# Performance work log

Measured on AMD Instinct MI355X. Metric: run time of the kernel, lower is better.

The kernel has to match this reference:

```python
import jax, jax.numpy as jnp
import numpy as np

B, N = 16384, 64

def setup_inputs() -> dict:
    key = jax.random.key(0)
    a = jax.random.normal(key, (B, N, N), dtype=jnp.float32)
    # symeig / eigh require symmetric input; symmetrize like SPD inputs would be
    x = 0.5 * (a + jnp.swapaxes(a, -2, -1))
    return {"input": x}

def reference(input) -> jnp.ndarray:
    # s, u = symeig(input); out = u @ diag(exp(s)) @ u^T
    s, u = jnp.linalg.eigh(input)          # s: [B,N], u: [B,N,N]
    # fuse diag_embed + two matmuls: (u * exp(s)) @ u^T
    return jnp.einsum('bik,bk,bjk->bij', u, jnp.exp(s), u)
```

## Files before the change

### kernel.cpp

```cpp
#include <hip/hip_runtime.h>
#include <math.h>

#define NB 64
#define TPB 256

__device__ __constant__ float CF[16] = {
    1.0f,
    1.0f,
    0.5f,
    1.6666666666666666e-01f,
    4.1666666666666664e-02f,
    8.3333333333333332e-03f,
    1.3888888888888889e-03f,
    1.9841269841269841e-04f,
    2.4801587301587302e-05f,
    2.7557319223985893e-06f,
    2.7557319223985888e-07f,
    2.5052108385441720e-08f,
    2.0876756987868100e-09f,
    1.6059043836821613e-10f,
    1.1470745597729725e-11f,
    7.6471637318198164e-13f
};

typedef __attribute__((ext_vector_type(8))) short bf16x8;
typedef __attribute__((ext_vector_type(16))) float f32x16;
typedef __attribute__((ext_vector_type(4))) unsigned int u32x4;

#define MFMA32 __builtin_amdgcn_mfma_f32_32x32x16_bf16
#define BCH(x) __builtin_bit_cast(bf16x8, x)

__device__ __forceinline__ void split_pk(float x0, float x1, unsigned& ph, unsigned& pl) {
    unsigned h;
    asm("v_cvt_pk_bf16_f32 %0, %1, %2" : "=v"(h) : "v"(x0), "v"(x1));
    float h0 = __builtin_bit_cast(float, h << 16);
    float h1 = __builtin_bit_cast(float, h & 0xFFFF0000u);
    float r0 = x0 - h0;
    float r1 = x1 - h1;
    unsigned l;
    asm("v_cvt_pk_bf16_f32 %0, %1, %2" : "=v"(l) : "v"(r0), "v"(r1));
    ph = h; pl = l;
}

__device__ __forceinline__ void pswap(unsigned& a, unsigned& b, int lh) {
#if __has_builtin(__builtin_amdgcn_permlane32_swap)
    auto r = __builtin_amdgcn_permlane32_swap((int)a, (int)b, false, false);
    a = (unsigned)r[0];
    b = (unsigned)r[1];
#else
    unsigned pa = (unsigned)__shfl_xor((int)a, 32);
    unsigned pb = (unsigned)__shfl_xor((int)b, 32);
    unsigned o0 = lh ? pb : a;
    unsigned o1 = lh ? b : pa;
    a = o0; b = o1;
#endif
}

__device__ __forceinline__ void tile_to_op(const float* v, int lh, u32x4* fh, u32x4* fl) {
    unsigned Wh[4][2], Wl[4][2];
#pragma unroll
    for (int g = 0; g < 4; ++g) {
        split_pk(v[g * 4 + 0], v[g * 4 + 1], Wh[g][0], Wl[g][0]);
        split_pk(v[g * 4 + 2], v[g * 4 + 3], Wh[g][1], Wl[g][1]);
    }
#pragma unroll
    for (int p = 0; p < 2; ++p) {
        unsigned a0 = Wh[2 * p][0], b0 = Wh[2 * p + 1][0];
        unsigned a1 = Wh[2 * p][1], b1 = Wh[2 * p + 1][1];
        pswap(a0, b0, lh);
        pswap(a1, b1, lh);
        fh[p] = (u32x4){a0, a1, b0, b1};
        a0 = Wl[2 * p][0]; b0 = Wl[2 * p + 1][0];
        a1 = Wl[2 * p][1]; b1 = Wl[2 * p + 1][1];
        pswap(a0, b0, lh);
        pswap(a1, b1, lh);
        fl[p] = (u32x4){a0, a1, b0, b1};
    }
}

__device__ __forceinline__ f32x16 mm3v(const u32x4* ah, const u32x4* al,
                                       const u32x4* bh, const u32x4* bl) {
    f32x16 acc = {};
#pragma unroll
    for (int f = 0; f < 4; ++f) acc = MFMA32(BCH(ah[f]), BCH(bh[f]), acc, 0, 0, 0);
#pragma unroll
    for (int f = 0; f < 4; ++f) acc = MFMA32(BCH(al[f]), BCH(bh[f]), acc, 0, 0, 0);
#pragma unroll
    for (int f = 0; f < 4; ++f) acc = MFMA32(BCH(ah[f]), BCH(bl[f]), acc, 0, 0, 0);
    return acc;
}

__device__ __forceinline__ void wr_tile(float* __restrict__ out, size_t base,
                                        int C, int R, int l31, int lh, const float* w) {
    float* rowp = out + base + (size_t)(C * 32 + l31) * NB + R * 32 + 4 * lh;
#pragma unroll
    for (int g = 0; g < 4; ++g) {
        float4 v = make_float4(w[g * 4 + 0], w[g * 4 + 1], w[g * 4 + 2], w[g * 4 + 3]);
        *reinterpret_cast<float4*>(rowp + 8 * g) = v;
    }
}

__global__ __launch_bounds__(TPB, 2)
void spd_expmap_reg(const float* __restrict__ in, float* __restrict__ out)
{
    const int tid  = threadIdx.x;
    const int lane = tid & 63;
    const int wv   = tid >> 6;
    const int l31 = lane & 31;
    const int lh  = lane >> 5;
    const size_t base = ((size_t)blockIdx.x * 4 + wv) * (NB * NB);
    const float* rp0 = in + base + (size_t)l31 * NB;
    const float* rp1 = rp0 + (size_t)32 * NB;

    unsigned dmask = 0;
#pragma unroll
    for (int g = 0; g < 4; ++g)
#pragma unroll
        for (int q = 0; q < 4; ++q)
            if (4 * lh + 8 * g + q == l31) dmask |= 1u << (g * 4 + q);

    u32x4 XH[2][4], XL[2][4];
#pragma unroll
    for (int R = 0; R < 2; ++R) {
        const float* rp = R ? rp1 : rp0;
#pragma unroll
        for (int f = 0; f < 4; ++f) {
            const float* q = rp + 16 * f + 8 * lh;
            float4 a = *reinterpret_cast<const float4*>(q);
            float4 b = *reinterpret_cast<const float4*>(q + 4);
            unsigned h0, l0, h1, l1, h2, l2, h3, l3;
            split_pk(a.x, a.y, h0, l0);
            split_pk(a.z, a.w, h1, l1);
            split_pk(b.x, b.y, h2, l2);
            split_pk(b.z, b.w, h3, l3);
            XH[R][f] = (u32x4){h0, h1, h2, h3};
            XL[R][f] = (u32x4){l0, l1, l2, l3};
        }
    }

    float x00[16], x10[16], x01[16], x11[16];
#pragma unroll
    for (int g = 0; g < 4; ++g) {
        float4 t;
        t = *reinterpret_cast<const float4*>(rp0 + 4 * lh + 8 * g);
        x00[g*4+0] = t.x; x00[g*4+1] = t.y; x00[g*4+2] = t.z; x00[g*4+3] = t.w;
        t = *reinterpret_cast<const float4*>(rp0 + 32 + 4 * lh + 8 * g);
        x10[g*4+0] = t.x; x10[g*4+1] = t.y; x10[g*4+2] = t.z; x10[g*4+3] = t.w;
        t = *reinterpret_cast<const float4*>(rp1 + 4 * lh + 8 * g);
        x01[g*4+0] = t.x; x01[g*4+1] = t.y; x01[g*4+2] = t.z; x01[g*4+3] = t.w;
        t = *reinterpret_cast<const float4*>(rp1 + 32 + 4 * lh + 8 * g);
        x11[g*4+0] = t.x; x11[g*4+1] = t.y; x11[g*4+2] = t.z; x11[g*4+3] = t.w;
    }

    f32x16 a00 = mm3v(XH[0], XL[0], XH[0], XL[0]);
    f32x16 a01 = mm3v(XH[0], XL[0], XH[1], XL[1]);
    f32x16 a10 = mm3v(XH[1], XL[1], XH[0], XL[0]);
    f32x16 a11 = mm3v(XH[1], XL[1], XH[1], XL[1]);

    float fr = 0.f;
#pragma unroll
    for (int r = 0; r < 16; ++r)
        fr += a00[r]*a00[r] + a01[r]*a01[r] + a10[r]*a10[r] + a11[r]*a11[r];
#pragma unroll
    for (int off = 32; off; off >>= 1) fr += __shfl_xor(fr, off);

    const float bound = sqrtf(sqrtf(fr));
    int sexp = 0;
    if (bound > 4.f) {
        sexp = (int)ceilf(log2f(bound)) - 2;
        if (sexp < 0) sexp = 0;
        if (sexp > 24) sexp = 24;
    }
    const float sc1 = exp2f(-(float)sexp);
    const float sc2 = sc1 * sc1;

#pragma unroll
    for (int r = 0; r < 16; ++r) { x00[r] *= sc1; x10[r] *= sc1; x01[r] *= sc1; x11[r] *= sc1; }

    u32x4 YH[2][4], YL[2][4];
    {
        float v[16];
#pragma unroll
        for (int r = 0; r < 16; ++r) v[r] = a00[r] * sc2;
        tile_to_op(v, lh, &YH[0][0], &YL[0][0]);
#pragma unroll
        for (int r = 0; r < 16; ++r) v[r] = a10[r] * sc2;
        tile_to_op(v, lh, &YH[0][2], &YL[0][2]);
#pragma unroll
        for (int r = 0; r < 16; ++r) v[r] = a01[r] * sc2;
        tile_to_op(v, lh, &YH[1][0], &YL[1][0]);
#pragma unroll
        for (int r = 0; r < 16; ++r) v[r] = a11[r] * sc2;
        tile_to_op(v, lh, &YH[1][2], &YL[1][2]);
    }

    u32x4 PH[2][4], PL[2][4];
    {
        float v[16];
#pragma unroll
        for (int r = 0; r < 16; ++r)
            v[r] = CF[13] * x00[r] + (((dmask >> r) & 1) ? CF[12] : 0.f);
        tile_to_op(v, lh, &PH[0][0], &PL[0][0]);
#pragma unroll
        for (int r = 0; r < 16; ++r) v[r] = CF[13] * x10[r];
        tile_to_op(v, lh, &PH[0][2], &PL[0][2]);
#pragma unroll
        for (int r = 0; r < 16; ++r) v[r] = CF[13] * x01[r];
        tile_to_op(v, lh, &PH[1][0], &PL[1][0]);
#pragma unroll
        for (int r = 0; r < 16; ++r)
            v[r] = CF[13] * x11[r] + (((dmask >> r) & 1) ? CF[12] : 0.f);
        tile_to_op(v, lh, &PH[1][2], &PL[1][2]);
    }

#pragma unroll 1
    for (int j = 5; j >= 0; --j) {
        const float cI = CF[2 * j], cX = CF[2 * j + 1];
        const bool last = (j == 0) && (sexp == 0);
        {
            f32x16 t0 = mm3v(YH[0], YL[0], PH[0], PL[0]);
            f32x16 t1 = mm3v(YH[1], YL[1], PH[0], PL[0]);
            float w0[16], w1[16];
#pragma unroll
            for (int r = 0; r < 16; ++r) {
                w0[r] = fmaf(cX, x00[r], t0[r]) + (((dmask >> r) & 1) ? cI : 0.f);
                w1[r] = fmaf(cX, x10[r], t1[r]);
            }
            if (last) {
                wr_tile(out, base, 0, 0, l31, lh, w0);
                wr_tile(out, base, 0, 1, l31, lh, w1);
            } else {
                tile_to_op(w0, lh, &PH[0][0], &PL[0][0]);
                tile_to_op(w1, lh, &PH[0][2], &PL[0][2]);
            }
        }
        {
            f32x16 t0 = mm3v(YH[0], YL[0], PH[1], PL[1]);
            f32x16 t1 = mm3v(YH[1], YL[1], PH[1], PL[1]);
            float w0[16], w1[16];
#pragma unroll
            for (int r = 0; r < 16; ++r) {
                w0[r] = fmaf(cX, x01[r], t0[r]);
                w1[r] = fmaf(cX, x11[r], t1[r]) + (((dmask >> r) & 1) ? cI : 0.f);
            }
            if (last) {
                wr_tile(out, base, 1, 0, l31, lh, w0);
                wr_tile(out, base, 1, 1, l31, lh, w1);
            } else {
                tile_to_op(w0, lh, &PH[1][0], &PL[1][0]);
                tile_to_op(w1, lh, &PH[1][2], &PL[1][2]);
            }
        }
    }

#pragma unroll 1
    for (int t = 0; t < sexp; ++t) {
        f32x16 s00 = mm3v(PH[0], PL[0], PH[0], PL[0]);
        f32x16 s01 = mm3v(PH[0], PL[0], PH[1], PL[1]);
        f32x16 s10 = mm3v(PH[1], PL[1], PH[0], PL[0]);
        f32x16 s11 = mm3v(PH[1], PL[1], PH[1], PL[1]);
        float w[16];
        if (t == sexp - 1) {
#pragma unroll
            for (int r = 0; r < 16; ++r) w[r] = s00[r];
            wr_tile(out, base, 0, 0, l31, lh, w);
#pragma unroll
            for (int r = 0; r < 16; ++r) w[r] = s10[r];
            wr_tile(out, base, 0, 1, l31, lh, w);
#pragma unroll
            for (int r = 0; r < 16; ++r) w[r] = s01[r];
            wr_tile(out, base, 1, 0, l31, lh, w);
#pragma unroll
            for (int r = 0; r < 16; ++r) w[r] = s11[r];
            wr_tile(out, base, 1, 1, l31, lh, w);
        } else {
#pragma unroll
            for (int r = 0; r < 16; ++r) w[r] = s00[r];
            tile_to_op(w, lh, &PH[0][0], &PL[0][0]);
#pragma unroll
            for (int r = 0; r < 16; ++r) w[r] = s10[r];
            tile_to_op(w, lh, &PH[0][2], &PL[0][2]);
#pragma unroll
            for (int r = 0; r < 16; ++r) w[r] = s01[r];
            tile_to_op(w, lh, &PH[1][0], &PL[1][0]);
#pragma unroll
            for (int r = 0; r < 16; ++r) w[r] = s11[r];
            tile_to_op(w, lh, &PH[1][2], &PL[1][2]);
        }
    }
}

extern "C" void kernel_launch(void* const* d_in, const int* in_sizes, int n_in,
                              void* d_out, int out_size, void* d_ws, size_t ws_size,
                              hipStream_t stream) {
    const float* in = reinterpret_cast<const float*>(d_in[0]);
    float* out = reinterpret_cast<float*>(d_out);
    const int nmat = in_sizes[0] / (NB * NB);
    hipLaunchKernelGGL(spd_expmap_reg, dim3(nmat / 4), dim3(TPB), 0, stream, in, out);
}
```

Before: 278.5 us.

## Re-read input tiles from global memory instead of holding them in registers

Drops the 64 persistent registers that held the scaled input matrix X and reloads X tiles from global memory (expected to hit cache) each time they are needed in the Taylor loop. The X² tiles are stored unscaled, and the scale factors are folded into the FMA coefficients so the pre-scaling passes disappear. Launch bounds rise from 2 to 3 blocks per CU to turn the lower register pressure into occupancy. The cost is repeated global loads inside the Horner loop and a risk of spills under the tighter register cap.

```diff
diff --git a/kernel.cpp b/kernel.cpp
--- a/kernel.cpp
+++ b/kernel.cpp
@@ -100,7 +100,16 @@
     }
 }
 
-__global__ __launch_bounds__(TPB, 2)
+__device__ __forceinline__ void load_x(const float* rp, int colbase, float* xr) {
+#pragma unroll
+    for (int g = 0; g < 4; ++g) {
+        float4 t = *reinterpret_cast<const float4*>(rp + colbase + 8 * g);
+        xr[g * 4 + 0] = t.x; xr[g * 4 + 1] = t.y;
+        xr[g * 4 + 2] = t.z; xr[g * 4 + 3] = t.w;
+    }
+}
+
+__global__ __launch_bounds__(TPB, 3)
 void spd_expmap_reg(const float* __restrict__ in, float* __restrict__ out)
 {
     const int tid  = threadIdx.x;
@@ -138,29 +147,27 @@
         }
     }
 
-    float x00[16], x10[16], x01[16], x11[16];
-#pragma unroll
-    for (int g = 0; g < 4; ++g) {
-        float4 t;
-        t = *reinterpret_cast<const float4*>(rp0 + 4 * lh + 8 * g);
-        x00[g*4+0] = t.x; x00[g*4+1] = t.y; x00[g*4+2] = t.z; x00[g*4+3] = t.w;
-        t = *reinterpret_cast<const float4*>(rp0 + 32 + 4 * lh + 8 * g);
-        x10[g*4+0] = t.x; x10[g*4+1] = t.y; x10[g*4+2] = t.z; x10[g*4+3] = t.w;
-        t = *reinterpret_cast<const float4*>(rp1 + 4 * lh + 8 * g);
-        x01[g*4+0] = t.x; x01[g*4+1] = t.y; x01[g*4+2] = t.z; x01[g*4+3] = t.w;
-        t = *reinterpret_cast<const float4*>(rp1 + 32 + 4 * lh + 8 * g);
-        x11[g*4+0] = t.x; x11[g*4+1] = t.y; x11[g*4+2] = t.z; x11[g*4+3] = t.w;
-    }
-
-    f32x16 a00 = mm3v(XH[0], XL[0], XH[0], XL[0]);
-    f32x16 a01 = mm3v(XH[0], XL[0], XH[1], XL[1]);
-    f32x16 a10 = mm3v(XH[1], XL[1], XH[0], XL[0]);
-    f32x16 a11 = mm3v(XH[1], XL[1], XH[1], XL[1]);
-
+    u32x4 YH[2][4], YL[2][4];
     float fr = 0.f;
-#pragma unroll
-    for (int r = 0; r < 16; ++r)
-        fr += a00[r]*a00[r] + a01[r]*a01[r] + a10[r]*a10[r] + a11[r]*a11[r];
+    {
+        f32x16 t;
+        t = mm3v(XH[0], XL[0], XH[0], XL[0]);
+#pragma unroll
+        for (int r = 0; r < 16; ++r) fr += t[r] * t[r];
+        tile_to_op((const float*)&t, lh, &YH[0][0], &YL[0][0]);
+        t = mm3v(XH[1], XL[1], XH[0], XL[0]);
+#pragma unroll
+        for (int r = 0; r < 16; ++r) fr += t[r] * t[r];
+        tile_to_op((const float*)&t, lh, &YH[0][2], &YL[0][2]);
+        t = mm3v(XH[0], XL[0], XH[1], XL[1]);
+#pragma unroll
+        for (int r = 0; r < 16; ++r) fr += t[r] * t[r];
+        tile_to_op((const float*)&t, lh, &YH[1][0], &YL[1][0]);
+        t = mm3v(XH[1], XL[1], XH[1], XL[1]);
+#pragma unroll
+        for (int r = 0; r < 16; ++r) fr += t[r] * t[r];
+        tile_to_op((const float*)&t, lh, &YH[1][2], &YL[1][2]);
+    }
 #pragma unroll
     for (int off = 32; off; off >>= 1) fr += __shfl_xor(fr, off);
 
@@ -174,82 +181,67 @@
     const float sc1 = exp2f(-(float)sexp);
     const float sc2 = sc1 * sc1;
 
-#pragma unroll
-    for (int r = 0; r < 16; ++r) { x00[r] *= sc1; x10[r] *= sc1; x01[r] *= sc1; x11[r] *= sc1; }
-
-    u32x4 YH[2][4], YL[2][4];
-    {
-        float v[16];
-#pragma unroll
-        for (int r = 0; r < 16; ++r) v[r] = a00[r] * sc2;
-        tile_to_op(v, lh, &YH[0][0], &YL[0][0]);
-#pragma unroll
-        for (int r = 0; r < 16; ++r) v[r] = a10[r] * sc2;
-        tile_to_op(v, lh, &YH[0][2], &YL[0][2]);
-#pragma unroll
-        for (int r = 0; r < 16; ++r) v[r] = a01[r] * sc2;
-        tile_to_op(v, lh, &YH[1][0], &YL[1][0]);
-#pragma unroll
-        for (int r = 0; r < 16; ++r) v[r] = a11[r] * sc2;
-        tile_to_op(v, lh, &YH[1][2], &YL[1][2]);
-    }
-
     u32x4 PH[2][4], PL[2][4];
     {
-        float v[16];
+        const float c13s = CF[13] * sc1;
+        float xr[16], w[16];
+        load_x(rp0, 4 * lh, xr);
 #pragma unroll
         for (int r = 0; r < 16; ++r)
-            v[r] = CF[13] * x00[r] + (((dmask >> r) & 1) ? CF[12] : 0.f);
-        tile_to_op(v, lh, &PH[0][0], &PL[0][0]);
-#pragma unroll
-        for (int r = 0; r < 16; ++r) v[r] = CF[13] * x10[r];
-        tile_to_op(v, lh, &PH[0][2], &PL[0][2]);
-#pragma unroll
-        for (int r = 0; r < 16; ++r) v[r] = CF[13] * x01[r];
-        tile_to_op(v, lh, &PH[1][0], &PL[1][0]);
+            w[r] = fmaf(c13s, xr[r], (((dmask >> r) & 1) ? CF[12] : 0.f));
+        tile_to_op(w, lh, &PH[0][0], &PL[0][0]);
+        load_x(rp0, 32 + 4 * lh, xr);
+#pragma unroll
+        for (int r = 0; r < 16; ++r) w[r] = c13s * xr[r];
+        tile_to_op(w, lh, &PH[0][2], &PL[0][2]);
+        load_x(rp1, 4 * lh, xr);
+#pragma unroll
+        for (int r = 0; r < 16; ++r) w[r] = c13s * xr[r];
+        tile_to_op(w, lh, &PH[1][0], &PL[1][0]);
+        load_x(rp1, 32 + 4 * lh, xr);
 #pragma unroll
         for (int r = 0; r < 16; ++r)
-            v[r] = CF[13] * x11[r] + (((dmask >> r) & 1) ? CF[12] : 0.f);
-        tile_to_op(v, lh, &PH[1][2], &PL[1][2]);
+            w[r] = fmaf(c13s, xr[r], (((dmask >> r) & 1) ? CF[12] : 0.f));
+        tile_to_op(w, lh, &PH[1][2], &PL[1][2]);
     }
 
 #pragma unroll 1
     for (int j = 5; j >= 0; --j) {
-        const float cI = CF[2 * j], cX = CF[2 * j + 1];
+        const float cI = CF[2 * j], cXs = CF[2 * j + 1] * sc1;
         const bool last = (j == 0) && (sexp == 0);
         {
             f32x16 t0 = mm3v(YH[0], YL[0], PH[0], PL[0]);
             f32x16 t1 = mm3v(YH[1], YL[1], PH[0], PL[0]);
-            float w0[16], w1[16];
-#pragma unroll
-            for (int r = 0; r < 16; ++r) {
-                w0[r] = fmaf(cX, x00[r], t0[r]) + (((dmask >> r) & 1) ? cI : 0.f);
-                w1[r] = fmaf(cX, x10[r], t1[r]);
-            }
-            if (last) {
-                wr_tile(out, base, 0, 0, l31, lh, w0);
-                wr_tile(out, base, 0, 1, l31, lh, w1);
-            } else {
-                tile_to_op(w0, lh, &PH[0][0], &PL[0][0]);
-                tile_to_op(w1, lh, &PH[0][2], &PL[0][2]);
-            }
+            float xr[16], w[16];
+            load_x(rp0, 4 * lh, xr);
+#pragma unroll
+            for (int r = 0; r < 16; ++r)
+                w[r] = fmaf(sc2, t0[r], fmaf(cXs, xr[r], (((dmask >> r) & 1) ? cI : 0.f)));
+            if (last) wr_tile(out, base, 0, 0, l31, lh, w);
+            else      tile_to_op(w, lh, &PH[0][0], &PL[0][0]);
+            load_x(rp0, 32 + 4 * lh, xr);
+#pragma unroll
+            for (int r = 0; r < 16; ++r)
+                w[r] = fmaf(sc2, t1[r], cXs * xr[r]);
+            if (last) wr_tile(out, base, 0, 1, l31, lh, w);
+            else      tile_to_op(w, lh, &PH[0][2], &PL[0][2]);
         }
         {
             f32x16 t0 = mm3v(YH[0], YL[0], PH[1], PL[1]);
             f32x16 t1 = mm3v(YH[1], YL[1], PH[1], PL[1]);
-            float w0[16], w1[16];
-#pragma unroll
-            for (int r = 0; r < 16; ++r) {
-                w0[r] = fmaf(cX, x01[r], t0[r]);
-                w1[r] = fmaf(cX, x11[r], t1[r]) + (((dmask >> r) & 1) ? cI : 0.f);
-            }
-            if (last) {
-                wr_tile(out, base, 1, 0, l31, lh, w0);
-                wr_tile(out, base, 1, 1, l31, lh, w1);
-            } else {
-                tile_to_op(w0, lh, &PH[1][0], &PL[1][0]);
-                tile_to_op(w1, lh, &PH[1][2], &PL[1][2]);
-            }
+            float xr[16], w[16];
+            load_x(rp1, 4 * lh, xr);
+#pragma unroll
+            for (int r = 0; r < 16; ++r)
+                w[r] = fmaf(sc2, t0[r], cXs * xr[r]);
+            if (last) wr_tile(out, base, 1, 0, l31, lh, w);
+            else      tile_to_op(w, lh, &PH[1][0], &PL[1][0]);
+            load_x(rp1, 32 + 4 * lh, xr);
+#pragma unroll
+            for (int r = 0; r < 16; ++r)
+                w[r] = fmaf(sc2, t1[r], fmaf(cXs, xr[r], (((dmask >> r) & 1) ? cI : 0.f)));
+            if (last) wr_tile(out, base, 1, 1, l31, lh, w);
+            else      tile_to_op(w, lh, &PH[1][2], &PL[1][2]);
         }
     }
 
@@ -259,33 +251,16 @@
         f32x16 s01 = mm3v(PH[0], PL[0], PH[1], PL[1]);
         f32x16 s10 = mm3v(PH[1], PL[1], PH[0], PL[0]);
         f32x16 s11 = mm3v(PH[1], PL[1], PH[1], PL[1]);
-        float w[16];
         if (t == sexp - 1) {
-#pragma unroll
-            for (int r = 0; r < 16; ++r) w[r] = s00[r];
-            wr_tile(out, base, 0, 0, l31, lh, w);
-#pragma unroll
-            for (int r = 0; r < 16; ++r) w[r] = s10[r];
-            wr_tile(out, base, 0, 1, l31, lh, w);
-#pragma unroll
-            for (int r = 0; r < 16; ++r) w[r] = s01[r];
-            wr_tile(out, base, 1, 0, l31, lh, w);
-#pragma unroll
-            for (int r = 0; r < 16; ++r) w[r] = s11[r];
-            wr_tile(out, base, 1, 1, l31, lh, w);
+            wr_tile(out, base, 0, 0, l31, lh, (const float*)&s00);
+            wr_tile(out, base, 0, 1, l31, lh, (const float*)&s10);
+            wr_tile(out, base, 1, 0, l31, lh, (const float*)&s01);
+            wr_tile(out, base, 1, 1, l31, lh, (const float*)&s11);
         } else {
-#pragma unroll
-            for (int r = 0; r < 16; ++r) w[r] = s00[r];
-            tile_to_op(w, lh, &PH[0][0], &PL[0][0]);
-#pragma unroll
-            for (int r = 0; r < 16; ++r) w[r] = s10[r];
-            tile_to_op(w, lh, &PH[0][2], &PL[0][2]);
-#pragma unroll
-            for (int r = 0; r < 16; ++r) w[r] = s01[r];
-            tile_to_op(w, lh, &PH[1][0], &PL[1][0]);
-#pragma unroll
-            for (int r = 0; r < 16; ++r) w[r] = s11[r];
-            tile_to_op(w, lh, &PH[1][2], &PL[1][2]);
+            tile_to_op((const float*)&s00, lh, &PH[0][0], &PL[0][0]);
+            tile_to_op((const float*)&s10, lh, &PH[0][2], &PL[0][2]);
+            tile_to_op((const float*)&s01, lh, &PH[1][0], &PL[1][0]);
+            tile_to_op((const float*)&s11, lh, &PH[1][2], &PL[1][2]);
         }
     }
 }
```

Result: slower. 654.5 us (+135.0%).
